# Kernel optimization log

Hardware: AMD Instinct MI355X
Metric: run time of the kernel (lower is better)

The kernel has to match this reference:

```python
import jax, jax.numpy as jnp
import numpy as np

H = 16        # num heads
NOPE = 128    # qk_nope_head_dim
ROPE = 64     # qk_rope_head_dim
VD = 128      # v_head_dim
HID = 2048    # hidden_dim
QLR = 1536    # q_lora_rank
KVLR = 512    # kv_lora_rank
B = 4
S = 1024
EPS = 1e-6


def setup_inputs() -> dict:
    key = jax.random.key(0)
    ks = jax.random.split(key, 8)
    def w(k, o, i):
        return jax.random.normal(k, (o, i), jnp.float32) * 0.02
    x = jax.random.normal(ks[0], (B * S, HID), jnp.float32)
    wq_a = w(ks[1], QLR, HID)
    w_qa_ln = jnp.ones((QLR,), jnp.float32)
    wq_b = w(ks[2], H * (NOPE + ROPE), QLR)
    wkv_a = w(ks[3], KVLR + ROPE, HID)
    w_kva_ln = jnp.ones((KVLR,), jnp.float32)
    wk_b = w(ks[4], H * NOPE, KVLR)
    wv_b = w(ks[5], H * VD, KVLR)
    wo = w(ks[6], HID, H * VD)
    # interleaved RoPE tables: [S, ROPE//2]
    pos = jnp.arange(S, dtype=jnp.float32)
    inv_freq = 1.0 / (10000.0 ** (jnp.arange(0, ROPE, 2, dtype=jnp.float32) / ROPE))
    freqs = pos[:, None] * inv_freq[None, :]
    rotary_sin = jnp.sin(freqs)
    rotary_cos = jnp.cos(freqs)
    seqstarts = jnp.arange(B + 1, dtype=jnp.int32) * S
    return dict(x=x, wq_a=wq_a, w_qa_ln=w_qa_ln, wq_b=wq_b, wkv_a=wkv_a,
                w_kva_ln=w_kva_ln, wk_b=wk_b, wv_b=wv_b, wo=wo,
                rotary_sin=rotary_sin, rotary_cos=rotary_cos, seqstarts=seqstarts)


def rmsnorm(h, w):
    return h * jax.lax.rsqrt(jnp.mean(h * h, axis=-1, keepdims=True) + EPS) * w


def rope_interleaved(t, sin, cos):
    # t: [B,S,h,ROPE]; sin/cos: [S,ROPE//2]; rotate adjacent pairs (even, odd)
    tr = t.reshape(t.shape[:-1] + (ROPE // 2, 2))
    e, o = tr[..., 0], tr[..., 1]
    s = sin[None, :, None, :]
    c = cos[None, :, None, :]
    return jnp.stack([e * c - o * s, e * s + o * c], axis=-1).reshape(t.shape)


def reference(x, wq_a, w_qa_ln, wq_b, wkv_a, w_kva_ln, wk_b, wv_b, wo,
              rotary_sin, rotary_cos, seqstarts):
    b = seqstarts.shape[0] - 1
    s = x.shape[0] // b
    # low-rank Q: hidden -> q_lora -> H*(nope+rope)
    q = rmsnorm(x @ wq_a.T, w_qa_ln) @ wq_b.T
    q = q.reshape(b, s, H, NOPE + ROPE)
    q_nope, q_pe = q[..., :NOPE], q[..., NOPE:]
    # low-rank KV: hidden -> kv_lora + rope (k_pe shared across heads)
    kv = x @ wkv_a.T
    ckv = rmsnorm(kv[:, :KVLR], w_kva_ln)
    k_pe = kv[:, KVLR:].reshape(b, s, 1, ROPE)
    k_nope = (ckv @ wk_b.T).reshape(b, s, H, NOPE)
    v = (ckv @ wv_b.T).reshape(b, s, H, VD)
    q_pe = rope_interleaved(q_pe, rotary_sin, rotary_cos)
    k_pe = rope_interleaved(k_pe, rotary_sin, rotary_cos)
    scale = 1.0 / np.sqrt(NOPE + ROPE).astype(np.float32)
    scores = (jnp.einsum('bqhd,bkhd->bhqk', q_nope, k_nope)
              + jnp.einsum('bqhd,bkjd->bhqk', q_pe, k_pe)) * scale
    causal = jnp.tril(jnp.ones((s, s), bool))
    scores = jnp.where(causal[None, None], scores, jnp.float32(-1e30))
    p = jax.nn.softmax(scores, axis=-1)
    out = jnp.einsum('bhqk,bkhd->bqhd', p, v).reshape(b * s, H * VD)
    return out @ wo.T
```

## Files before the change

### kernel.cpp

```cpp
#include <hip/hip_runtime.h>
#include <stdint.h>

typedef __bf16 bf16;
typedef __bf16 bf16x8 __attribute__((ext_vector_type(8)));
typedef float floatx4 __attribute__((ext_vector_type(4)));

#define HH     16
#define DNOPE  128
#define DROPE  64
#define DV     128
#define DQK    192
#define HID    2048
#define QLR    1536
#define KVLR   512
#define BB     4
#define SS     1024
#define NTOK   4096
#define XOUTW  2176
#define EPSF   1e-6f

__device__ inline void cvt_store4(bf16* dst, float a, float b, float c, float d) {
  union { bf16 h[4]; uint2 u; } t;
  t.h[0] = (bf16)a; t.h[1] = (bf16)b; t.h[2] = (bf16)c; t.h[3] = (bf16)d;
  *(uint2*)dst = t.u;
}

__device__ inline void gl_lds16(const bf16* g, bf16* l) {
  __builtin_amdgcn_global_load_lds(
      (const __attribute__((address_space(1))) void*)g,
      (__attribute__((address_space(3))) void*)l, 16, 0, 0);
}

__global__ __launch_bounds__(256) void cvt_all(
    const float* __restrict__ x, const float* __restrict__ wq_a,
    const float* __restrict__ wkv_a, const float* __restrict__ wq_b,
    const float* __restrict__ wk_b, const float* __restrict__ wv_b,
    const float* __restrict__ wo, bf16* __restrict__ xb,
    bf16* __restrict__ wA, bf16* __restrict__ wqbb,
    bf16* __restrict__ wkvB, bf16* __restrict__ wob, float scaleq) {
  const int blk = blockIdx.x, tid = threadIdx.x;
  const float* s; bf16* d; int rel; float sc = 1.0f;
  if (blk < 8192)       { rel = blk;         s = x;    d = xb; }
  else if (blk < 11264) { rel = blk - 8192;  s = wq_a; d = wA; }
  else if (blk < 12544) {
    rel = blk - 11264;
    int i = (rel * 256 + tid) << 2;
    bf16* dd = wA + 3145728;
    if ((i >> 11) < 576) {
      float4 v = *(const float4*)(wkv_a + i);
      cvt_store4(dd + i, v.x, v.y, v.z, v.w);
    } else {
      *(uint2*)(dd + i) = make_uint2(0u, 0u);
    }
    return;
  }
  else if (blk < 17152) { rel = blk - 12544; s = wq_b; d = wqbb; sc = scaleq; }
  else if (blk < 18176) { rel = blk - 17152; s = wk_b; d = wkvB; }
  else if (blk < 19200) { rel = blk - 18176; s = wv_b; d = wkvB + 1048576; }
  else                  { rel = blk - 19200; s = wo;   d = wob; }
  int i = (rel * 256 + tid) << 2;
  float4 v = *(const float4*)(s + i);
  cvt_store4(d + i, v.x * sc, v.y * sc, v.z * sc, v.w * sc);
}

template <typename TC, int EPI>
__global__ __launch_bounds__(256) void gemm_bt_bf16(
    const bf16* __restrict__ A, const bf16* __restrict__ Bw,
    TC* __restrict__ C0, bf16* __restrict__ C1, int M, int N, int K) {
  __shared__ __align__(16) bf16 As[128 * 64];
  __shared__ __align__(16) bf16 Bs[128 * 64];
  const int tid  = threadIdx.x;
  const int wave = tid >> 6, lane = tid & 63;
  const int m0 = blockIdx.x << 7, n0 = blockIdx.y << 7;
  const int quad = lane >> 4, l16 = lane & 15;
  const int wm = (wave >> 1) << 6, wn = (wave & 1) << 6;
  const int srow = wave << 5;
  const int lrow = lane >> 3;
  const int lcol = (lane & 7) << 3;

  const bf16* gA = A  + (size_t)(m0 + srow + lrow) * K + lcol;
  const bf16* gB = Bw + (size_t)(n0 + srow + lrow) * K + lcol;
  bf16* lA = As + srow * 64;
  bf16* lB = Bs + srow * 64;

  floatx4 acc[4][4];
#pragma unroll
  for (int i = 0; i < 4; i++)
#pragma unroll
    for (int j = 0; j < 4; j++) acc[i][j] = floatx4{0.f, 0.f, 0.f, 0.f};

  for (int k0 = 0; k0 < K; k0 += 64) {
    __syncthreads();
#pragma unroll
    for (int t = 0; t < 4; t++) {
      gl_lds16(gA + (size_t)(t << 3) * K + k0, lA + (t << 3) * 64);
      gl_lds16(gB + (size_t)(t << 3) * K + k0, lB + (t << 3) * 64);
    }
    __syncthreads();
#pragma unroll
    for (int ks = 0; ks < 2; ks++) {
      bf16x8 af[4], bv[4];
#pragma unroll
      for (int i = 0; i < 4; i++)
        af[i] = *(const bf16x8*)&As[(wm + (i << 4) + l16) * 64 + (ks << 5) + (quad << 3)];
#pragma unroll
      for (int j = 0; j < 4; j++)
        bv[j] = *(const bf16x8*)&Bs[(wn + (j << 4) + l16) * 64 + (ks << 5) + (quad << 3)];
#pragma unroll
      for (int i = 0; i < 4; i++)
#pragma unroll
        for (int j = 0; j < 4; j++)
          acc[i][j] = __builtin_amdgcn_mfma_f32_16x16x32_bf16(af[i], bv[j], acc[i][j], 0, 0, 0);
    }
  }

  if constexpr (EPI == 1) {
    if (n0 >= 2048) {
#pragma unroll
      for (int i = 0; i < 4; i++) {
        int gm = m0 + wm + (i << 4) + (quad << 2);
        int bb = gm >> 10, s = gm & 1023;
#pragma unroll
        for (int j = 0; j < 4; j++) {
          int gn = n0 + wn + (j << 4) + l16 - 2048;
          int hh = gn >> 7, vd = gn & 127;
          union { bf16 h4[4]; uint2 u; } pk;
#pragma unroll
          for (int r = 0; r < 4; r++) pk.h4[r] = (bf16)acc[i][j][r];
          *(uint2*)(C1 + ((((size_t)bb * HH + hh) * DV + vd) << 10) + s) = pk.u;
        }
      }
      return;
    }
  }
  const int ldc = (EPI == 1) ? 2048 : N;
#pragma unroll
  for (int i = 0; i < 4; i++)
#pragma unroll
    for (int j = 0; j < 4; j++) {
      int gn = n0 + wn + (j << 4) + l16;
#pragma unroll
      for (int r = 0; r < 4; r++) {
        int gm = m0 + wm + (i << 4) + (quad << 2) + r;
        C0[(size_t)gm * ldc + gn] = (TC)acc[i][j][r];
      }
    }
}

__global__ __launch_bounds__(256) void norm_rope(
    const bf16* __restrict__ xout, const float* __restrict__ w_qa_ln,
    const float* __restrict__ w_kva_ln, bf16* __restrict__ qln,
    bf16* __restrict__ ckv, bf16* __restrict__ kpe,
    const float* __restrict__ rsin, const float* __restrict__ rcos) {
  const int blk = blockIdx.x, tid = threadIdx.x;
  if (blk < 8192) {
    const int row = blk & 4095;
    const bool isq = blk < 4096;
    const bf16* p = xout + (size_t)row * XOUTW + (isq ? 0 : QLR);
    const float* w = isq ? w_qa_ln : w_kva_ln;
    bf16* o = isq ? (qln + (size_t)row * QLR) : (ckv + (size_t)row * KVLR);
    const int L = isq ? QLR : KVLR;
    float ss = 0.f;
    for (int c = tid << 2; c < L; c += 1024) {
      union { uint2 u; bf16 h[4]; } t;
      t.u = *(const uint2*)(p + c);
#pragma unroll
      for (int r = 0; r < 4; r++) { float v = (float)t.h[r]; ss += v * v; }
    }
#pragma unroll
    for (int off = 32; off > 0; off >>= 1) ss += __shfl_down(ss, off);
    __shared__ float red[4];
    if ((tid & 63) == 0) red[tid >> 6] = ss;
    __syncthreads();
    float rs = rsqrtf((red[0] + red[1] + red[2] + red[3]) / (float)L + EPSF);
    for (int c = tid << 2; c < L; c += 1024) {
      union { uint2 u; bf16 h[4]; } t, ot;
      t.u = *(const uint2*)(p + c);
#pragma unroll
      for (int r = 0; r < 4; r++) ot.h[r] = (bf16)((float)t.h[r] * rs * w[c + r]);
      *(uint2*)(o + c) = ot.u;
    }
  } else {
    int idx = (blk - 8192) * 256 + tid;
    int i = idx & 31, row = idx >> 5;
    int pos = row & (SS - 1);
    union { uint u; bf16 h2[2]; } t;
    t.u = *(const uint*)(xout + (size_t)row * XOUTW + QLR + KVLR + (i << 1));
    float e = (float)t.h2[0], o = (float)t.h2[1];
    float c = rcos[(pos << 5) + i], s = rsin[(pos << 5) + i];
    t.h2[0] = (bf16)(e * c - o * s);
    t.h2[1] = (bf16)(e * s + o * c);
    *(uint*)(kpe + (size_t)row * DROPE + (i << 1)) = t.u;
  }
}

__global__ void rope_q(bf16* __restrict__ q, const float* __restrict__ sin_t,
                       const float* __restrict__ cos_t) {
  int idx = blockIdx.x * 256 + threadIdx.x;
  int i = idx & 31, h = (idx >> 5) & 15, row = idx >> 9;
  int pos = row & (SS - 1);
  bf16* base = q + ((size_t)row * HH + h) * DQK + DNOPE + (i << 1);
  union { uint u; bf16 h2[2]; } t;
  t.u = *(uint*)base;
  float e = (float)t.h2[0], o = (float)t.h2[1];
  float c = cos_t[(pos << 5) + i], s = sin_t[(pos << 5) + i];
  t.h2[0] = (bf16)(e * c - o * s);
  t.h2[1] = (bf16)(e * s + o * c);
  *(uint*)base = t.u;
}

__global__ __launch_bounds__(512) void attn_kernel(
    const bf16* __restrict__ q, const bf16* __restrict__ knope,
    const bf16* __restrict__ kpe, const bf16* __restrict__ vT,
    bf16* __restrict__ out) {
  const int qt = 7 - blockIdx.x;
  const int q0 = qt << 7;
  const int nkt = (qt << 1) + 2;
  const int h = blockIdx.y, b = blockIdx.z;
  __shared__ __align__(16) bf16 smem[40960];
  __shared__ __align__(16) bf16 Ps[8][16][72];
  __shared__ float alphaS[8][16], invlS[8][16];
  const int tid = threadIdx.x, wave = tid >> 6, lane = tid & 63;
  const int quad = lane >> 4, l16 = lane & 15;

  const bf16 *gkn0, *gkn1, *gkp, *gvt0, *gvt1;
  {
    int c = wave << 1;
    int r = (c << 2) + (lane >> 4);
    int bi = (lane & 15) ^ (r & 15);
    gkn0 = knope + ((size_t)((b << 10) + r) * HH + h) * DNOPE + (bi << 3);
    r = ((c + 1) << 2) + (lane >> 4);
    bi = (lane & 15) ^ (r & 15);
    gkn1 = knope + ((size_t)((b << 10) + r) * HH + h) * DNOPE + (bi << 3);
    r = (wave << 3) + (lane >> 3);
    bi = (lane & 7) ^ (r & 7);
    gkp = kpe + (size_t)((b << 10) + r) * DROPE + (bi << 3);
    int dv = (wave << 4) + (lane >> 3);
    bi = (lane & 7) ^ (dv & 7);
    gvt0 = vT + ((((size_t)b * HH + h) * DV + dv) << 10) + (bi << 3);
    dv += 8;
    bi = (lane & 7) ^ (dv & 7);
    gvt1 = vT + ((((size_t)b * HH + h) * DV + dv) << 10) + (bi << 3);
  }
  const size_t knstep = (size_t)64 * HH * DNOPE;
  const size_t kpstep = (size_t)64 * DROPE;
  const int woff = wave << 10, woff2 = wave << 9;

  {
    bf16* bufp = smem;
    gl_lds16(gkn0, bufp + woff);
    gl_lds16(gkn1, bufp + woff + 512);
    gl_lds16(gkp,  bufp + 8192 + woff2);
    gl_lds16(gvt0, bufp + 12288 + woff);
    gl_lds16(gvt1, bufp + 12288 + woff + 512);
    gkn0 += knstep; gkn1 += knstep; gkp += kpstep; gvt0 += 64; gvt1 += 64;
  }

  bf16x8 aq[6];
  bf16* qov = smem + 20480;
  for (int round = 0; round < 2; round++) {
    __syncthreads();
    for (int i = tid; i < 64 * 24; i += 512) {
      int r = i / 24, c = (i % 24) << 3;
      *(uint4*)&qov[r * 200 + c] = *(const uint4*)(
          q + ((size_t)((b << 10) + q0 + (round << 6) + r) * HH + h) * DQK + c);
    }
    __syncthreads();
    if ((wave >> 2) == round) {
      int rw = wave & 3;
#pragma unroll
      for (int t = 0; t < 6; t++)
        aq[t] = *(const bf16x8*)&qov[((rw << 4) + l16) * 200 + (t << 5) + (quad << 3)];
    }
  }
  asm volatile("s_waitcnt lgkmcnt(0)" ::: "memory");

  floatx4 acc_o[8];
#pragma unroll
  for (int n = 0; n < 8; n++) acc_o[n] = floatx4{0.f, 0.f, 0.f, 0.f};
  float m_i[4], l_i[4];
#pragma unroll
  for (int r = 0; r < 4; r++) { m_i[r] = -1e30f; l_i[r] = 0.f; }

  for (int s = 0; s < nkt; s++) {
    asm volatile("s_waitcnt vmcnt(0)\n\ts_barrier" ::: "memory");
    if (s + 1 < nkt) {
      bf16* bufp = smem + ((s + 1) & 1) * 20480;
      gl_lds16(gkn0, bufp + woff);
      gl_lds16(gkn1, bufp + woff + 512);
      gl_lds16(gkp,  bufp + 8192 + woff2);
      gl_lds16(gvt0, bufp + 12288 + woff);
      gl_lds16(gvt1, bufp + 12288 + woff + 512);
      gkn0 += knstep; gkn1 += knstep; gkp += kpstep; gvt0 += 64; gvt1 += 64;
    }
    __builtin_amdgcn_sched_barrier(0);

    const bf16* Kn = smem + (s & 1) * 20480;
    const bf16* Kp = Kn + 8192;
    const bf16* Vt = Kn + 12288;

    floatx4 sacc[4];
#pragma unroll
    for (int kn = 0; kn < 4; kn++) {
      floatx4 sc = floatx4{0.f, 0.f, 0.f, 0.f};
#pragma unroll
      for (int t = 0; t < 4; t++) {
        int sbi = ((t << 2) + quad) ^ l16;
        bf16x8 bk = *(const bf16x8*)&Kn[(((kn << 4) + l16) << 7) + (sbi << 3)];
        sc = __builtin_amdgcn_mfma_f32_16x16x32_bf16(aq[t], bk, sc, 0, 0, 0);
      }
#pragma unroll
      for (int t = 0; t < 2; t++) {
        int sbi = ((t << 2) + quad) ^ (l16 & 7);
        bf16x8 bk = *(const bf16x8*)&Kp[(((kn << 4) + l16) << 6) + (sbi << 3)];
        sc = __builtin_amdgcn_mfma_f32_16x16x32_bf16(aq[4 + t], bk, sc, 0, 0, 0);
      }
      sacc[kn] = sc;
    }

    const int k0 = s << 6;
    float pvv[4][4], mtile[4];
#pragma unroll
    for (int r = 0; r < 4; r++) mtile[r] = -1e30f;
    if (s >= nkt - 2) {
#pragma unroll
      for (int kn = 0; kn < 4; kn++)
#pragma unroll
        for (int r = 0; r < 4; r++) {
          int qg = q0 + (wave << 4) + (quad << 2) + r;
          int kg = k0 + (kn << 4) + l16;
          float sv = sacc[kn][r];
          if (kg > qg) sv = -1e30f;
          pvv[kn][r] = sv;
          mtile[r] = fmaxf(mtile[r], sv);
        }
    } else {
#pragma unroll
      for (int kn = 0; kn < 4; kn++)
#pragma unroll
        for (int r = 0; r < 4; r++) {
          float sv = sacc[kn][r];
          pvv[kn][r] = sv;
          mtile[r] = fmaxf(mtile[r], sv);
        }
    }
    float alpha[4];
#pragma unroll
    for (int r = 0; r < 4; r++) {
#pragma unroll
      for (int off = 1; off < 16; off <<= 1)
        mtile[r] = fmaxf(mtile[r], __shfl_xor(mtile[r], off));
      float mnew = fmaxf(m_i[r], mtile[r]);
      alpha[r] = exp2f(m_i[r] - mnew);
      m_i[r] = mnew;
      float part = 0.f;
#pragma unroll
      for (int kn = 0; kn < 4; kn++) {
        float p = exp2f(pvv[kn][r] - mnew);
        pvv[kn][r] = p;
        part += p;
      }
#pragma unroll
      for (int off = 1; off < 16; off <<= 1) part += __shfl_xor(part, off);
      l_i[r] = l_i[r] * alpha[r] + part;
    }
#pragma unroll
    for (int kn = 0; kn < 4; kn++)
#pragma unroll
      for (int r = 0; r < 4; r++)
        Ps[wave][(quad << 2) + r][(kn << 4) + l16] = (bf16)pvv[kn][r];
    if (l16 == 0)
      *(float4*)&alphaS[wave][quad << 2] =
          make_float4(alpha[0], alpha[1], alpha[2], alpha[3]);
    float alpha_lane = alphaS[wave][l16];
#pragma unroll
    for (int n = 0; n < 8; n++)
#pragma unroll
      for (int r = 0; r < 4; r++) acc_o[n][r] *= alpha_lane;

    bf16x8 bp[2];
#pragma unroll
    for (int t = 0; t < 2; t++)
      bp[t] = *(const bf16x8*)&Ps[wave][l16][(t << 5) + (quad << 3)];
#pragma unroll
    for (int n = 0; n < 8; n++) {
#pragma unroll
      for (int t = 0; t < 2; t++) {
        int sbi = ((t << 2) + quad) ^ (l16 & 7);
        bf16x8 av = *(const bf16x8*)&Vt[(((n << 4) + l16) << 6) + (sbi << 3)];
        acc_o[n] = __builtin_amdgcn_mfma_f32_16x16x32_bf16(av, bp[t], acc_o[n], 0, 0, 0);
      }
    }
  }

  if (l16 == 0)
    *(float4*)&invlS[wave][quad << 2] =
        make_float4(1.f / l_i[0], 1.f / l_i[1], 1.f / l_i[2], 1.f / l_i[3]);
  asm volatile("s_waitcnt lgkmcnt(0)\n\ts_barrier" ::: "memory");
  float invl = invlS[wave][l16];
  int tok = (b << 10) + q0 + (wave << 4) + l16;
  bf16* obase = out + ((size_t)tok * HH + h) * DV + (quad << 2);
#pragma unroll
  for (int n = 0; n < 8; n++) {
    union { bf16 h4[4]; uint2 u; } pk;
#pragma unroll
    for (int r = 0; r < 4; r++) pk.h4[r] = (bf16)(acc_o[n][r] * invl);
    *(uint2*)(obase + (n << 4)) = pk.u;
  }
}

extern "C" void kernel_launch(void* const* d_in, const int* in_sizes, int n_in,
                              void* d_out, int out_size, void* d_ws, size_t ws_size,
                              hipStream_t stream) {
  (void)in_sizes; (void)n_in; (void)out_size; (void)ws_size;
  const float* x        = (const float*)d_in[0];
  const float* wq_a     = (const float*)d_in[1];
  const float* w_qa_ln  = (const float*)d_in[2];
  const float* wq_b     = (const float*)d_in[3];
  const float* wkv_a    = (const float*)d_in[4];
  const float* w_kva_ln = (const float*)d_in[5];
  const float* wk_b     = (const float*)d_in[6];
  const float* wv_b     = (const float*)d_in[7];
  const float* wo       = (const float*)d_in[8];
  const float* rsin     = (const float*)d_in[9];
  const float* rcos     = (const float*)d_in[10];
  float* out = (float*)d_out;

  char* ws = (char*)d_ws;
  bf16* xb    = (bf16*)(ws + 0);
  bf16* attnb = (bf16*)(ws + 0);
  bf16* xout  = (bf16*)(ws + 16777216);
  bf16* knope = (bf16*)(ws + 16777216);
  bf16* q     = (bf16*)(ws + 34603008);
  bf16* qln   = (bf16*)(ws + 59768832);
  bf16* vT    = (bf16*)(ws + 59768832);
  bf16* wA    = (bf16*)(ws + 76546048);
  bf16* wqbb  = (bf16*)(ws + 85458944);
  bf16* wkvB  = (bf16*)(ws + 94896128);
  bf16* wob   = (bf16*)(ws + 99090432);
  bf16* ckv   = (bf16*)(ws + 107479040);
  bf16* kpe   = (bf16*)(ws + 111673344);

  const float SCALEQ = (1.0f / sqrtf(192.0f)) * 1.44269504088896f;

  dim3 blk(256);
  cvt_all<<<23296, blk, 0, stream>>>(x, wq_a, wkv_a, wq_b, wk_b, wv_b, wo,
                                     xb, wA, wqbb, wkvB, wob, SCALEQ);
  gemm_bt_bf16<bf16, 0><<<dim3(32, 17), blk, 0, stream>>>(
      xb, wA, xout, nullptr, NTOK, XOUTW, HID);
  norm_rope<<<8704, blk, 0, stream>>>(xout, w_qa_ln, w_kva_ln, qln, ckv, kpe,
                                      rsin, rcos);
  gemm_bt_bf16<bf16, 0><<<dim3(32, 24), blk, 0, stream>>>(
      qln, wqbb, q, nullptr, NTOK, HH * DQK, QLR);
  rope_q<<<8192, blk, 0, stream>>>(q, rsin, rcos);
  gemm_bt_bf16<bf16, 1><<<dim3(32, 32), blk, 0, stream>>>(
      ckv, wkvB, knope, vT, NTOK, 4096, KVLR);
  attn_kernel<<<dim3(8, HH, BB), dim3(512), 0, stream>>>(
      q, knope, kpe, vT, attnb);
  gemm_bt_bf16<float, 0><<<dim3(32, 16), blk, 0, stream>>>(
      attnb, wob, out, nullptr, NTOK, HID, HID);
}
```

Measured before the change: 491.0 us.

## Single-buffer V tile, halve P staging, and raise attention kernel occupancy

The attention kernel now double-buffers only the K tiles and keeps V in a single LDS buffer that is loaded at the start of each iteration and waited on with a partial vmcnt before the PV step. The P staging buffer is halved, and the PV product is split into two 32-column halves that reuse it. Lower LDS use plus launch_bounds(512,4) aims to fit more blocks per CU, and s_setprio is raised around the MFMA sections. The V load is no longer prefetched a full iteration ahead, so its latency is less hidden, and the final barrier before reading invlS was dropped.

New measurement: 491.6 us. No clear change (+0.1%).

```diff
diff --git a/kernel.cpp b/kernel.cpp
--- a/kernel.cpp
+++ b/kernel.cpp
@@ -209,7 +209,7 @@
   *(uint*)base = t.u;
 }
 
-__global__ __launch_bounds__(512) void attn_kernel(
+__global__ __launch_bounds__(512, 4) void attn_kernel(
     const bf16* __restrict__ q, const bf16* __restrict__ knope,
     const bf16* __restrict__ kpe, const bf16* __restrict__ vT,
     bf16* __restrict__ out) {
@@ -217,8 +217,8 @@
   const int q0 = qt << 7;
   const int nkt = (qt << 1) + 2;
   const int h = blockIdx.y, b = blockIdx.z;
-  __shared__ __align__(16) bf16 smem[40960];
-  __shared__ __align__(16) bf16 Ps[8][16][72];
+  __shared__ __align__(16) bf16 smem[32768];
+  __shared__ __align__(16) bf16 Ps[8][16][40];
   __shared__ float alphaS[8][16], invlS[8][16];
   const int tid = threadIdx.x, wave = tid >> 6, lane = tid & 63;
   const int quad = lane >> 4, l16 = lane & 15;
@@ -246,24 +246,19 @@
   const size_t kpstep = (size_t)64 * DROPE;
   const int woff = wave << 10, woff2 = wave << 9;
 
-  {
-    bf16* bufp = smem;
-    gl_lds16(gkn0, bufp + woff);
-    gl_lds16(gkn1, bufp + woff + 512);
-    gl_lds16(gkp,  bufp + 8192 + woff2);
-    gl_lds16(gvt0, bufp + 12288 + woff);
-    gl_lds16(gvt1, bufp + 12288 + woff + 512);
-    gkn0 += knstep; gkn1 += knstep; gkp += kpstep; gvt0 += 64; gvt1 += 64;
-  }
+  gl_lds16(gkn0, smem + woff);
+  gl_lds16(gkn1, smem + woff + 512);
+  gl_lds16(gkp,  smem + 8192 + woff2);
+  gkn0 += knstep; gkn1 += knstep; gkp += kpstep;
 
   bf16x8 aq[6];
-  bf16* qov = smem + 20480;
+  bf16* qov = smem + 12288;
   for (int round = 0; round < 2; round++) {
     __syncthreads();
     for (int i = tid; i < 64 * 24; i += 512) {
-      int r = i / 24, c = (i % 24) << 3;
-      *(uint4*)&qov[r * 200 + c] = *(const uint4*)(
-          q + ((size_t)((b << 10) + q0 + (round << 6) + r) * HH + h) * DQK + c);
+      int r = i / 24, cc = (i % 24) << 3;
+      *(uint4*)&qov[r * 200 + cc] = *(const uint4*)(
+          q + ((size_t)((b << 10) + q0 + (round << 6) + r) * HH + h) * DQK + cc);
     }
     __syncthreads();
     if ((wave >> 2) == round) {
@@ -284,22 +279,23 @@
 
   for (int s = 0; s < nkt; s++) {
     asm volatile("s_waitcnt vmcnt(0)\n\ts_barrier" ::: "memory");
+    gl_lds16(gvt0, smem + 24576 + woff);
+    gl_lds16(gvt1, smem + 24576 + woff + 512);
+    gvt0 += 64; gvt1 += 64;
     if (s + 1 < nkt) {
-      bf16* bufp = smem + ((s + 1) & 1) * 20480;
+      bf16* bufp = smem + ((s + 1) & 1) * 12288;
       gl_lds16(gkn0, bufp + woff);
       gl_lds16(gkn1, bufp + woff + 512);
       gl_lds16(gkp,  bufp + 8192 + woff2);
-      gl_lds16(gvt0, bufp + 12288 + woff);
-      gl_lds16(gvt1, bufp + 12288 + woff + 512);
-      gkn0 += knstep; gkn1 += knstep; gkp += kpstep; gvt0 += 64; gvt1 += 64;
+      gkn0 += knstep; gkn1 += knstep; gkp += kpstep;
     }
     __builtin_amdgcn_sched_barrier(0);
 
-    const bf16* Kn = smem + (s & 1) * 20480;
+    const bf16* Kn = smem + (s & 1) * 12288;
     const bf16* Kp = Kn + 8192;
-    const bf16* Vt = Kn + 12288;
 
     floatx4 sacc[4];
+    __builtin_amdgcn_s_setprio(1);
 #pragma unroll
     for (int kn = 0; kn < 4; kn++) {
       floatx4 sc = floatx4{0.f, 0.f, 0.f, 0.f};
@@ -317,6 +313,7 @@
       }
       sacc[kn] = sc;
     }
+    __builtin_amdgcn_s_setprio(0);
 
     const int k0 = s << 6;
     float pvv[4][4], mtile[4];
@@ -364,11 +361,7 @@
       for (int off = 1; off < 16; off <<= 1) part += __shfl_xor(part, off);
       l_i[r] = l_i[r] * alpha[r] + part;
     }
-#pragma unroll
-    for (int kn = 0; kn < 4; kn++)
-#pragma unroll
-      for (int r = 0; r < 4; r++)
-        Ps[wave][(quad << 2) + r][(kn << 4) + l16] = (bf16)pvv[kn][r];
+
     if (l16 == 0)
       *(float4*)&alphaS[wave][quad << 2] =
           make_float4(alpha[0], alpha[1], alpha[2], alpha[3]);
@@ -378,25 +371,47 @@
 #pragma unroll
       for (int r = 0; r < 4; r++) acc_o[n][r] *= alpha_lane;
 
-    bf16x8 bp[2];
-#pragma unroll
-    for (int t = 0; t < 2; t++)
-      bp[t] = *(const bf16x8*)&Ps[wave][l16][(t << 5) + (quad << 3)];
+#pragma unroll
+    for (int knl = 0; knl < 2; knl++)
+#pragma unroll
+      for (int r = 0; r < 4; r++)
+        Ps[wave][(quad << 2) + r][(knl << 4) + l16] = (bf16)pvv[knl][r];
+
+    if (s + 1 < nkt)
+      asm volatile("s_waitcnt vmcnt(3)\n\ts_barrier" ::: "memory");
+    else
+      asm volatile("s_waitcnt vmcnt(0)\n\ts_barrier" ::: "memory");
+
+    const bf16* Vt = smem + 24576;
+    bf16x8 bp = *(const bf16x8*)&Ps[wave][l16][quad << 3];
+    __builtin_amdgcn_s_setprio(1);
 #pragma unroll
     for (int n = 0; n < 8; n++) {
-#pragma unroll
-      for (int t = 0; t < 2; t++) {
-        int sbi = ((t << 2) + quad) ^ (l16 & 7);
-        bf16x8 av = *(const bf16x8*)&Vt[(((n << 4) + l16) << 6) + (sbi << 3)];
-        acc_o[n] = __builtin_amdgcn_mfma_f32_16x16x32_bf16(av, bp[t], acc_o[n], 0, 0, 0);
-      }
-    }
+      int sbi = quad ^ (l16 & 7);
+      bf16x8 av = *(const bf16x8*)&Vt[(((n << 4) + l16) << 6) + (sbi << 3)];
+      acc_o[n] = __builtin_amdgcn_mfma_f32_16x16x32_bf16(av, bp, acc_o[n], 0, 0, 0);
+    }
+    __builtin_amdgcn_s_setprio(0);
+#pragma unroll
+    for (int knl = 0; knl < 2; knl++)
+#pragma unroll
+      for (int r = 0; r < 4; r++)
+        Ps[wave][(quad << 2) + r][(knl << 4) + l16] = (bf16)pvv[2 + knl][r];
+    bp = *(const bf16x8*)&Ps[wave][l16][quad << 3];
+    __builtin_amdgcn_s_setprio(1);
+#pragma unroll
+    for (int n = 0; n < 8; n++) {
+      int sbi = (4 + quad) ^ (l16 & 7);
+      bf16x8 av = *(const bf16x8*)&Vt[(((n << 4) + l16) << 6) + (sbi << 3)];
+      acc_o[n] = __builtin_amdgcn_mfma_f32_16x16x32_bf16(av, bp, acc_o[n], 0, 0, 0);
+    }
+    __builtin_amdgcn_s_setprio(0);
   }
 
   if (l16 == 0)
     *(float4*)&invlS[wave][quad << 2] =
         make_float4(1.f / l_i[0], 1.f / l_i[1], 1.f / l_i[2], 1.f / l_i[3]);
-  asm volatile("s_waitcnt lgkmcnt(0)\n\ts_barrier" ::: "memory");
+  asm volatile("s_waitcnt lgkmcnt(0)" ::: "memory");
   float invl = invlS[wave][l16];
   int tok = (b << 10) + q0 + (wave << 4) + l16;
   bf16* obase = out + ((size_t)tok * HH + h) * DV + (quad << 2);
```

## Rewrite attention with 32x32 MFMA, 256-row query tiles and register-only P exchange

Applied to the files above, without the earlier changes.

The attention kernel now uses 32x32x16 MFMA instructions. Each wave owns 32 query rows, and a block covers 256 queries, so the grid halves. Q is loaded straight into registers instead of being staged through shared memory. The P tile is kept in registers and rearranged with cross-lane shuffles rather than written to shared memory, and the online-softmax rescale is skipped when the running max grows by no more than 8. In exchange, fewer blocks are launched, waves whose rows are fully masked sit idle through some tiles, and register pressure rises under the new launch bounds.

Result: faster. 452.8 us (-7.8%).

```diff
diff --git a/kernel.cpp b/kernel.cpp
--- a/kernel.cpp
+++ b/kernel.cpp
@@ -4,6 +4,7 @@
 typedef __bf16 bf16;
 typedef __bf16 bf16x8 __attribute__((ext_vector_type(8)));
 typedef float floatx4 __attribute__((ext_vector_type(4)));
+typedef float floatx16 __attribute__((ext_vector_type(16)));
 
 #define HH     16
 #define DNOPE  128
@@ -209,19 +210,20 @@
   *(uint*)base = t.u;
 }
 
-__global__ __launch_bounds__(512) void attn_kernel(
+__global__ __launch_bounds__(512, 2) void attn_kernel(
     const bf16* __restrict__ q, const bf16* __restrict__ knope,
     const bf16* __restrict__ kpe, const bf16* __restrict__ vT,
     bf16* __restrict__ out) {
-  const int qt = 7 - blockIdx.x;
-  const int q0 = qt << 7;
-  const int nkt = (qt << 1) + 2;
+  const int qt = 3 - blockIdx.x;
+  const int q0 = qt << 8;
+  const int nkt = (qt + 1) << 2;
   const int h = blockIdx.y, b = blockIdx.z;
   __shared__ __align__(16) bf16 smem[40960];
-  __shared__ __align__(16) bf16 Ps[8][16][72];
-  __shared__ float alphaS[8][16], invlS[8][16];
   const int tid = threadIdx.x, wave = tid >> 6, lane = tid & 63;
-  const int quad = lane >> 4, l16 = lane & 15;
+  const int l32 = lane & 31, hi = lane >> 5;
+  const int hi4 = hi << 2;
+  const int Q0w = q0 + (wave << 5);
+  const int qg = Q0w + l32;
 
   const bf16 *gkn0, *gkn1, *gkp, *gvt0, *gvt1;
   {
@@ -246,43 +248,31 @@
   const size_t kpstep = (size_t)64 * DROPE;
   const int woff = wave << 10, woff2 = wave << 9;
 
+  gl_lds16(gkn0, smem + woff);
+  gl_lds16(gkn1, smem + woff + 512);
+  gl_lds16(gkp,  smem + 8192 + woff2);
+  gl_lds16(gvt0, smem + 12288 + woff);
+  gl_lds16(gvt1, smem + 12288 + woff + 512);
+  gkn0 += knstep; gkn1 += knstep; gkp += kpstep; gvt0 += 64; gvt1 += 64;
+
+  bf16x8 qb[12];
   {
-    bf16* bufp = smem;
-    gl_lds16(gkn0, bufp + woff);
-    gl_lds16(gkn1, bufp + woff + 512);
-    gl_lds16(gkp,  bufp + 8192 + woff2);
-    gl_lds16(gvt0, bufp + 12288 + woff);
-    gl_lds16(gvt1, bufp + 12288 + woff + 512);
-    gkn0 += knstep; gkn1 += knstep; gkp += kpstep; gvt0 += 64; gvt1 += 64;
-  }
-
-  bf16x8 aq[6];
-  bf16* qov = smem + 20480;
-  for (int round = 0; round < 2; round++) {
-    __syncthreads();
-    for (int i = tid; i < 64 * 24; i += 512) {
-      int r = i / 24, c = (i % 24) << 3;
-      *(uint4*)&qov[r * 200 + c] = *(const uint4*)(
-          q + ((size_t)((b << 10) + q0 + (round << 6) + r) * HH + h) * DQK + c);
-    }
-    __syncthreads();
-    if ((wave >> 2) == round) {
-      int rw = wave & 3;
-#pragma unroll
-      for (int t = 0; t < 6; t++)
-        aq[t] = *(const bf16x8*)&qov[((rw << 4) + l16) * 200 + (t << 5) + (quad << 3)];
-    }
-  }
-  asm volatile("s_waitcnt lgkmcnt(0)" ::: "memory");
-
-  floatx4 acc_o[8];
-#pragma unroll
-  for (int n = 0; n < 8; n++) acc_o[n] = floatx4{0.f, 0.f, 0.f, 0.f};
-  float m_i[4], l_i[4];
-#pragma unroll
-  for (int r = 0; r < 4; r++) { m_i[r] = -1e30f; l_i[r] = 0.f; }
+    const bf16* qbase =
+        q + ((size_t)((b << 10) + Q0w + l32) * HH + h) * DQK + (hi << 3);
+#pragma unroll
+    for (int dc = 0; dc < 12; dc++)
+      qb[dc] = *(const bf16x8*)(qbase + (dc << 4));
+  }
+
+  floatx16 acc[4];
+#pragma unroll
+  for (int g = 0; g < 4; g++)
+#pragma unroll
+    for (int r = 0; r < 16; r++) acc[g][r] = 0.f;
+  float m_i = -1e30f, l_i = 0.f;
 
   for (int s = 0; s < nkt; s++) {
+    const int k0 = s << 6;
     asm volatile("s_waitcnt vmcnt(0)\n\ts_barrier" ::: "memory");
     if (s + 1 < nkt) {
       bf16* bufp = smem + ((s + 1) & 1) * 20480;
@@ -294,119 +284,122 @@
       gkn0 += knstep; gkn1 += knstep; gkp += kpstep; gvt0 += 64; gvt1 += 64;
     }
     __builtin_amdgcn_sched_barrier(0);
+    if (k0 > Q0w + 31) continue;
 
     const bf16* Kn = smem + (s & 1) * 20480;
     const bf16* Kp = Kn + 8192;
     const bf16* Vt = Kn + 12288;
 
-    floatx4 sacc[4];
-#pragma unroll
-    for (int kn = 0; kn < 4; kn++) {
-      floatx4 sc = floatx4{0.f, 0.f, 0.f, 0.f};
-#pragma unroll
-      for (int t = 0; t < 4; t++) {
-        int sbi = ((t << 2) + quad) ^ l16;
-        bf16x8 bk = *(const bf16x8*)&Kn[(((kn << 4) + l16) << 7) + (sbi << 3)];
-        sc = __builtin_amdgcn_mfma_f32_16x16x32_bf16(aq[t], bk, sc, 0, 0, 0);
-      }
-#pragma unroll
-      for (int t = 0; t < 2; t++) {
-        int sbi = ((t << 2) + quad) ^ (l16 & 7);
-        bf16x8 bk = *(const bf16x8*)&Kp[(((kn << 4) + l16) << 6) + (sbi << 3)];
-        sc = __builtin_amdgcn_mfma_f32_16x16x32_bf16(aq[4 + t], bk, sc, 0, 0, 0);
-      }
-      sacc[kn] = sc;
-    }
-
-    const int k0 = s << 6;
-    float pvv[4][4], mtile[4];
-#pragma unroll
-    for (int r = 0; r < 4; r++) mtile[r] = -1e30f;
-    if (s >= nkt - 2) {
-#pragma unroll
-      for (int kn = 0; kn < 4; kn++)
-#pragma unroll
-        for (int r = 0; r < 4; r++) {
-          int qg = q0 + (wave << 4) + (quad << 2) + r;
-          int kg = k0 + (kn << 4) + l16;
-          float sv = sacc[kn][r];
-          if (kg > qg) sv = -1e30f;
-          pvv[kn][r] = sv;
-          mtile[r] = fmaxf(mtile[r], sv);
-        }
-    } else {
-#pragma unroll
-      for (int kn = 0; kn < 4; kn++)
-#pragma unroll
-        for (int r = 0; r < 4; r++) {
-          float sv = sacc[kn][r];
-          pvv[kn][r] = sv;
-          mtile[r] = fmaxf(mtile[r], sv);
-        }
-    }
-    float alpha[4];
-#pragma unroll
-    for (int r = 0; r < 4; r++) {
-#pragma unroll
-      for (int off = 1; off < 16; off <<= 1)
-        mtile[r] = fmaxf(mtile[r], __shfl_xor(mtile[r], off));
-      float mnew = fmaxf(m_i[r], mtile[r]);
-      alpha[r] = exp2f(m_i[r] - mnew);
-      m_i[r] = mnew;
-      float part = 0.f;
-#pragma unroll
-      for (int kn = 0; kn < 4; kn++) {
-        float p = exp2f(pvv[kn][r] - mnew);
-        pvv[kn][r] = p;
-        part += p;
-      }
-#pragma unroll
-      for (int off = 1; off < 16; off <<= 1) part += __shfl_xor(part, off);
-      l_i[r] = l_i[r] * alpha[r] + part;
-    }
-#pragma unroll
-    for (int kn = 0; kn < 4; kn++)
+    floatx16 s0, s1;
+#pragma unroll
+    for (int r = 0; r < 16; r++) { s0[r] = 0.f; s1[r] = 0.f; }
+    __builtin_amdgcn_s_setprio(1);
+#pragma unroll
+    for (int dc = 0; dc < 12; dc++) {
+      bf16x8 ak0, ak1;
+      if (dc < 8) {
+        int gi = (((dc << 1) + hi) ^ (l32 & 15)) << 3;
+        ak0 = *(const bf16x8*)&Kn[(l32 << 7) + gi];
+        ak1 = *(const bf16x8*)&Kn[((32 + l32) << 7) + gi];
+      } else {
+        int gi = ((((dc - 8) << 1) + hi) ^ (l32 & 7)) << 3;
+        ak0 = *(const bf16x8*)&Kp[(l32 << 6) + gi];
+        ak1 = *(const bf16x8*)&Kp[((32 + l32) << 6) + gi];
+      }
+      s0 = __builtin_amdgcn_mfma_f32_32x32x16_bf16(ak0, qb[dc], s0, 0, 0, 0);
+      s1 = __builtin_amdgcn_mfma_f32_32x32x16_bf16(ak1, qb[dc], s1, 0, 0, 0);
+    }
+    __builtin_amdgcn_s_setprio(0);
+
+    if (k0 + 63 > Q0w) {
+#pragma unroll
+      for (int r = 0; r < 16; r++) {
+        int rp = (r & 3) + ((r >> 2) << 3) + hi4;
+        if (k0 + rp > qg)      s0[r] = -1e30f;
+        if (k0 + 32 + rp > qg) s1[r] = -1e30f;
+      }
+    }
+
+    float mx = -1e30f;
+#pragma unroll
+    for (int r = 0; r < 16; r++) mx = fmaxf(mx, fmaxf(s0[r], s1[r]));
+    mx = fmaxf(mx, __shfl_xor(mx, 32));
+    if (!__all(mx - m_i <= 8.0f)) {
+      float mnew = fmaxf(m_i, mx);
+      float alpha = exp2f(m_i - mnew);
+      l_i *= alpha;
+#pragma unroll
+      for (int g = 0; g < 4; g++)
+#pragma unroll
+        for (int r = 0; r < 16; r++) acc[g][r] *= alpha;
+      m_i = mnew;
+    }
+    float sum = 0.f;
+#pragma unroll
+    for (int r = 0; r < 16; r++) {
+      float p0 = exp2f(s0[r] - m_i), p1 = exp2f(s1[r] - m_i);
+      s0[r] = p0; s1[r] = p1;
+      sum += p0 + p1;
+    }
+    sum += __shfl_xor(sum, 32);
+    l_i += sum;
+
+    uint P32[2][4][2];
+#pragma unroll
+    for (int hh = 0; hh < 4; hh++) {
+      union { bf16 e[2]; uint u; } w0, w1, w2, w3;
+      w0.e[0] = (bf16)s0[(hh << 2) + 0]; w0.e[1] = (bf16)s0[(hh << 2) + 1];
+      w1.e[0] = (bf16)s0[(hh << 2) + 2]; w1.e[1] = (bf16)s0[(hh << 2) + 3];
+      w2.e[0] = (bf16)s1[(hh << 2) + 0]; w2.e[1] = (bf16)s1[(hh << 2) + 1];
+      w3.e[0] = (bf16)s1[(hh << 2) + 2]; w3.e[1] = (bf16)s1[(hh << 2) + 3];
+      P32[0][hh][0] = w0.u; P32[0][hh][1] = w1.u;
+      P32[1][hh][0] = w2.u; P32[1][hh][1] = w3.u;
+    }
+    bf16x8 bp[4];
+#pragma unroll
+    for (int c = 0; c < 4; c++) {
+      const int t = c >> 1, sb = c & 1;
+      uint send0 = hi ? P32[t][(sb << 1)][0] : P32[t][(sb << 1) + 1][0];
+      uint send1 = hi ? P32[t][(sb << 1)][1] : P32[t][(sb << 1) + 1][1];
+      uint r0 = __shfl_xor(send0, 32);
+      uint r1 = __shfl_xor(send1, 32);
+      union { uint u[4]; bf16x8 v; } f;
+      if (hi == 0) {
+        f.u[0] = P32[t][(sb << 1)][0]; f.u[1] = P32[t][(sb << 1)][1];
+        f.u[2] = r0;                   f.u[3] = r1;
+      } else {
+        f.u[0] = r0;                         f.u[1] = r1;
+        f.u[2] = P32[t][(sb << 1) + 1][0];   f.u[3] = P32[t][(sb << 1) + 1][1];
+      }
+      bp[c] = f.v;
+    }
+
+    __builtin_amdgcn_s_setprio(1);
+#pragma unroll
+    for (int c = 0; c < 4; c++) {
+      const int gsw = (((c << 1) + hi) ^ (l32 & 7)) << 3;
+#pragma unroll
+      for (int g = 0; g < 4; g++) {
+        bf16x8 av = *(const bf16x8*)&Vt[(((g << 5) + l32) << 6) + gsw];
+        acc[g] = __builtin_amdgcn_mfma_f32_32x32x16_bf16(av, bp[c], acc[g], 0, 0, 0);
+      }
+    }
+    __builtin_amdgcn_s_setprio(0);
+  }
+
+  const float invl = 1.0f / l_i;
+  const int tok = (b << 10) + Q0w + l32;
+  bf16* obase = out + ((size_t)tok * HH + h) * DV + hi4;
+#pragma unroll
+  for (int g = 0; g < 4; g++)
+#pragma unroll
+    for (int t = 0; t < 4; t++) {
+      union { bf16 h4[4]; uint2 u; } pk;
 #pragma unroll
       for (int r = 0; r < 4; r++)
-        Ps[wave][(quad << 2) + r][(kn << 4) + l16] = (bf16)pvv[kn][r];
-    if (l16 == 0)
-      *(float4*)&alphaS[wave][quad << 2] =
-          make_float4(alpha[0], alpha[1], alpha[2], alpha[3]);
-    float alpha_lane = alphaS[wave][l16];
-#pragma unroll
-    for (int n = 0; n < 8; n++)
-#pragma unroll
-      for (int r = 0; r < 4; r++) acc_o[n][r] *= alpha_lane;
-
-    bf16x8 bp[2];
-#pragma unroll
-    for (int t = 0; t < 2; t++)
-      bp[t] = *(const bf16x8*)&Ps[wave][l16][(t << 5) + (quad << 3)];
-#pragma unroll
-    for (int n = 0; n < 8; n++) {
-#pragma unroll
-      for (int t = 0; t < 2; t++) {
-        int sbi = ((t << 2) + quad) ^ (l16 & 7);
-        bf16x8 av = *(const bf16x8*)&Vt[(((n << 4) + l16) << 6) + (sbi << 3)];
-        acc_o[n] = __builtin_amdgcn_mfma_f32_16x16x32_bf16(av, bp[t], acc_o[n], 0, 0, 0);
-      }
-    }
-  }
-
-  if (l16 == 0)
-    *(float4*)&invlS[wave][quad << 2] =
-        make_float4(1.f / l_i[0], 1.f / l_i[1], 1.f / l_i[2], 1.f / l_i[3]);
-  asm volatile("s_waitcnt lgkmcnt(0)\n\ts_barrier" ::: "memory");
-  float invl = invlS[wave][l16];
-  int tok = (b << 10) + q0 + (wave << 4) + l16;
-  bf16* obase = out + ((size_t)tok * HH + h) * DV + (quad << 2);
-#pragma unroll
-  for (int n = 0; n < 8; n++) {
-    union { bf16 h4[4]; uint2 u; } pk;
-#pragma unroll
-    for (int r = 0; r < 4; r++) pk.h4[r] = (bf16)(acc_o[n][r] * invl);
-    *(uint2*)(obase + (n << 4)) = pk.u;
-  }
+        pk.h4[r] = (bf16)(acc[g][(t << 2) + r] * invl);
+      *(uint2*)(obase + (g << 5) + (t << 3)) = pk.u;
+    }
 }
 
 extern "C" void kernel_launch(void* const* d_in, const int* in_sizes, int n_in,
@@ -455,7 +448,7 @@
   rope_q<<<8192, blk, 0, stream>>>(q, rsin, rcos);
   gemm_bt_bf16<bf16, 1><<<dim3(32, 32), blk, 0, stream>>>(
       ckv, wkvB, knope, vT, NTOK, 4096, KVLR);
-  attn_kernel<<<dim3(8, HH, BB), dim3(512), 0, stream>>>(
+  attn_kernel<<<dim3(4, HH, BB), dim3(512), 0, stream>>>(
       q, knope, kpe, vT, attnb);
   gemm_bt_bf16<float, 0><<<dim3(32, 16), blk, 0, stream>>>(
       attnb, wob, out, nullptr, NTOK, HID, HID);
```
